# Kernel optimization log

Hardware: AMD Instinct MI355X
Metric: run time of the kernel (lower is better)

The kernel has to match this reference:

```python
import jax, jax.numpy as jnp
import numpy as np

WINDOW = 128
STRIDE = 16

def setup_inputs() -> dict:
    key = jax.random.key(0)
    input_data = jax.random.normal(key, (16, 4096, 128), dtype=jnp.float32)
    return {"input_data": input_data}

def reference(input_data) -> jnp.ndarray:
    B, T, F = input_data.shape
    num_windows = (T - WINDOW) // STRIDE + 1  # 249
    # time indices for every window: [num_windows, WINDOW]
    idx = jnp.arange(num_windows)[:, None] * STRIDE + jnp.arange(WINDOW)[None, :]
    # gather overlapping windows: [B, num_windows, WINDOW, F]
    windows = input_data[:, idx, :]
    # per-window X^T X / WINDOW: [B, num_windows, F, F]
    pccs = jnp.einsum('bwlf,bwlg->bwfg', windows, windows) / WINDOW
    return pccs
```

## Files before the change

kernel.cpp:

```cpp
#include <hip/hip_runtime.h>

#define WINDOW 128
#define STRIDE 16
#define NWIN   249
#define NF     128
#define SEQ    4096
#define LROWS  160

typedef _Float16 f16;
typedef _Float16 f16x2 __attribute__((ext_vector_type(2)));
typedef _Float16 f16x8 __attribute__((ext_vector_type(8)));
typedef float    f32x4 __attribute__((ext_vector_type(4)));
typedef float    f32x16 __attribute__((ext_vector_type(16)));

union V8 { f16x8 v8; f16x2 v2[4]; };

__device__ __forceinline__ void stage8(const float* __restrict__ src, f16* lds,
                                       int f0, int l0) {
    f32x4 rows[8];
    #pragma unroll
    for (int j = 0; j < 8; ++j)
        rows[j] = *(const f32x4*)&src[(size_t)(l0 + j) * NF + f0];
    const int cbase = l0 >> 3;
    #pragma unroll
    for (int d = 0; d < 4; ++d) {
        const int f = f0 + d;
        V8 u;
        #pragma unroll
        for (int jj = 0; jj < 4; ++jj) {
            auto p = __builtin_amdgcn_cvt_pkrtz(rows[2 * jj][d], rows[2 * jj + 1][d]);
            u.v2[jj] = *(f16x2*)&p;
        }
        u.v8 = u.v8 * (f16)0.08838834764831845f;
        const int ch = (l0 < 128) ? (cbase ^ (f & 15))
                                  : (16 + ((cbase & 3) ^ (f & 3)));
        *(f16x8*)&lds[f * LROWS + ch * 8] = u.v8;
    }
}

template<int CO>
__device__ __forceinline__ void compute_and_store(const f16* lds, int lane,
                                                  int wr, int wc, float* __restrict__ dst) {
    const int c15 = lane & 15;
    const int c31 = lane & 31;
    const int h   = lane >> 5;

    f32x16 acc[2][2];
    #pragma unroll
    for (int i = 0; i < 2; ++i)
        #pragma unroll
        for (int j = 0; j < 2; ++j)
            acc[i][j] = (f32x16)(0.0f);

    #pragma unroll
    for (int ks = 0; ks < 8; ++ks) {
        const int clog = CO + 2 * ks + h;
        int pc;
        if (CO == 0 || CO + 2 * ks + 1 < 16)
            pc = clog ^ c15;
        else
            pc = 16 + ((clog & 3) ^ (lane & 3));
        const int off = pc * 8;

        f16x8 af[2], bf[2];
        #pragma unroll
        for (int i = 0; i < 2; ++i)
            af[i] = *(const f16x8*)&lds[(64 * wr + 32 * i + c31) * LROWS + off];
        #pragma unroll
        for (int j = 0; j < 2; ++j)
            bf[j] = *(const f16x8*)&lds[(64 * wc + 32 * j + c31) * LROWS + off];

        #pragma unroll
        for (int i = 0; i < 2; ++i)
            #pragma unroll
            for (int j = 0; j < 2; ++j)
                acc[i][j] = __builtin_amdgcn_mfma_f32_32x32x16_f16(af[i], bf[j], acc[i][j], 0, 0, 0);
    }

    #pragma unroll
    for (int i = 0; i < 2; ++i) {
        const int R0 = 64 * wr + 32 * i + 4 * h;
        #pragma unroll
        for (int j = 0; j < 2; ++j) {
            float* dcol = dst + 64 * wc + 32 * j + c31;
            #pragma unroll
            for (int reg = 0; reg < 16; ++reg) {
                const int row = R0 + (reg & 3) + 8 * (reg >> 2);
                __builtin_nontemporal_store(acc[i][j][reg], &dcol[(size_t)row * NF]);
            }
        }
    }
}

__global__ __launch_bounds__(256, 4) void pcc_kernel(const float* __restrict__ in,
                                                     float* __restrict__ out) {
    __shared__ f16 lds[NF * LROWS];

    const int lin = blockIdx.x + 125 * blockIdx.y;
    const int swz = (lin & 7) * 250 + (lin >> 3);
    const int wp  = swz % 125;
    const int b   = swz / 125;

    const int tid = threadIdx.x;
    const bool full = (wp < 124);
    const int stage_base = full ? 32 * wp : (SEQ - 144);

    const float* src = in + ((size_t)b * SEQ + stage_base) * NF;
    const int f0 = 4 * (tid & 31);
    const int lh = tid >> 5;

    stage8(src, lds, f0, 8 * lh);
    stage8(src, lds, f0, 64 + 8 * lh);
    if (tid < 64)
        stage8(src, lds, f0, 128 + 8 * lh);
    __syncthreads();

    const int lane = tid & 63;
    const int wid  = tid >> 6;
    const int wr   = wid >> 1;
    const int wc   = wid & 1;

    float* outb = out + (size_t)b * NWIN * (NF * NF);
    if (full)
        compute_and_store<0>(lds, lane, wr, wc, outb + (size_t)(2 * wp) * (NF * NF));
    const int w1 = full ? (2 * wp + 1) : (NWIN - 1);
    compute_and_store<2>(lds, lane, wr, wc, outb + (size_t)w1 * (NF * NF));
}

extern "C" void kernel_launch(void* const* d_in, const int* in_sizes, int n_in,
                              void* d_out, int out_size, void* d_ws, size_t ws_size,
                              hipStream_t stream) {
    (void)in_sizes; (void)n_in; (void)d_ws; (void)ws_size; (void)out_size;
    const float* in = (const float*)d_in[0];
    float* out = (float*)d_out;
    dim3 grid(125, 16);
    pcc_kernel<<<grid, dim3(256, 1, 1), 0, stream>>>(in, out);
}
```

Measured before the change: 296.7 us.

## Process four windows per block using a ring LDS buffer with overlapped staging

Each block now covers a 64-row strip and computes four consecutive windows instead of two, staging 160 rows up front and then streaming the next 16 rows into a circular LDS buffer while earlier windows compute. This halves the number of blocks and reduces redundant global loads and f16 conversion of overlapping input rows. The LDS swizzle is simplified to XOR within groups of four chunks to support the wraparound. In exchange, the grid is smaller (63x16), which may lower occupancy and parallelism, and extra barriers are added inside the block.

```diff
diff --git a/kernel.cpp b/kernel.cpp
--- a/kernel.cpp
+++ b/kernel.cpp
@@ -6,22 +6,26 @@
 #define NF     128
 #define SEQ    4096
 #define LROWS  160
+#define NSTRIP 63
 
 typedef _Float16 f16;
 typedef _Float16 f16x2 __attribute__((ext_vector_type(2)));
+typedef _Float16 f16x4 __attribute__((ext_vector_type(4)));
 typedef _Float16 f16x8 __attribute__((ext_vector_type(8)));
 typedef float    f32x4 __attribute__((ext_vector_type(4)));
 typedef float    f32x16 __attribute__((ext_vector_type(16)));
 
 union V8 { f16x8 v8; f16x2 v2[4]; };
+union V4 { f16x4 v4; f16x2 v2[2]; };
+
 
 __device__ __forceinline__ void stage8(const float* __restrict__ src, f16* lds,
-                                       int f0, int l0) {
+                                       int f0, int l0 ) {
     f32x4 rows[8];
     #pragma unroll
     for (int j = 0; j < 8; ++j)
         rows[j] = *(const f32x4*)&src[(size_t)(l0 + j) * NF + f0];
-    const int cbase = l0 >> 3;
+    const int ch = l0 >> 3;
     #pragma unroll
     for (int d = 0; d < 4; ++d) {
         const int f = f0 + d;
@@ -32,18 +36,43 @@
             u.v2[jj] = *(f16x2*)&p;
         }
         u.v8 = u.v8 * (f16)0.08838834764831845f;
-        const int ch = (l0 < 128) ? (cbase ^ (f & 15))
-                                  : (16 + ((cbase & 3) ^ (f & 3)));
-        *(f16x8*)&lds[f * LROWS + ch * 8] = u.v8;
+        const int pch = (ch & ~3) | ((ch ^ (f >> 1)) & 3);
+        *(f16x8*)&lds[f * LROWS + pch * 8] = u.v8;
     }
 }
 
-template<int CO>
-__device__ __forceinline__ void compute_and_store(const f16* lds, int lane,
-                                                  int wr, int wc, float* __restrict__ dst) {
-    const int c15 = lane & 15;
+__device__ __forceinline__ void load4(const float* __restrict__ src, f32x4 r[4],
+                                      int f0, int l0) {
+    #pragma unroll
+    for (int j = 0; j < 4; ++j)
+        r[j] = *(const f32x4*)&src[(size_t)(l0 + j) * NF + f0];
+}
+
+__device__ __forceinline__ void write4(f16* lds, const f32x4 r[4], int f0, int relrow) {
+    const int phys = relrow - (relrow >= LROWS ? LROWS : 0);
+    const int ch = phys >> 3;
+    const int sub = phys & 7;
+    #pragma unroll
+    for (int d = 0; d < 4; ++d) {
+        const int f = f0 + d;
+        V4 u;
+        {
+            auto p0 = __builtin_amdgcn_cvt_pkrtz(r[0][d], r[1][d]);
+            auto p1 = __builtin_amdgcn_cvt_pkrtz(r[2][d], r[3][d]);
+            u.v2[0] = *(f16x2*)&p0;
+            u.v2[1] = *(f16x2*)&p1;
+        }
+        u.v4 = u.v4 * (f16)0.08838834764831845f;
+        const int pch = (ch & ~3) | ((ch ^ (f >> 1)) & 3);
+        *(f16x4*)&lds[f * LROWS + pch * 8 + sub] = u.v4;
+    }
+}
+
+__device__ __forceinline__ void compute_store(const f16* lds, int lane, int wr, int wc,
+                                              int wi, float* __restrict__ dst) {
     const int c31 = lane & 31;
     const int h   = lane >> 5;
+    const int q2  = c31 >> 1;
 
     f32x16 acc[2][2];
     #pragma unroll
@@ -52,29 +81,26 @@
         for (int j = 0; j < 2; ++j)
             acc[i][j] = (f32x16)(0.0f);
 
+    const int fa0 = (64 * wr + c31) * LROWS;
+    const int fa1 = (64 * wr + 32 + c31) * LROWS;
+    const int fb0 = (64 * wc + c31) * LROWS;
+    const int fb1 = (64 * wc + 32 + c31) * LROWS;
+
     #pragma unroll
     for (int ks = 0; ks < 8; ++ks) {
-        const int clog = CO + 2 * ks + h;
-        int pc;
-        if (CO == 0 || CO + 2 * ks + 1 < 16)
-            pc = clog ^ c15;
-        else
-            pc = 16 + ((clog & 3) ^ (lane & 3));
-        const int off = pc * 8;
+        const int chlog = 2 * wi + 2 * ks + h;
+        const int ch = chlog - (chlog >= 20 ? 20 : 0);
+        const int off = ((ch & ~3) | ((ch ^ q2) & 3)) * 8;
 
-        f16x8 af[2], bf[2];
-        #pragma unroll
-        for (int i = 0; i < 2; ++i)
-            af[i] = *(const f16x8*)&lds[(64 * wr + 32 * i + c31) * LROWS + off];
-        #pragma unroll
-        for (int j = 0; j < 2; ++j)
-            bf[j] = *(const f16x8*)&lds[(64 * wc + 32 * j + c31) * LROWS + off];
+        const f16x8 a0 = *(const f16x8*)&lds[fa0 + off];
+        const f16x8 a1 = *(const f16x8*)&lds[fa1 + off];
+        const f16x8 b0 = *(const f16x8*)&lds[fb0 + off];
+        const f16x8 b1 = *(const f16x8*)&lds[fb1 + off];
 
-        #pragma unroll
-        for (int i = 0; i < 2; ++i)
-            #pragma unroll
-            for (int j = 0; j < 2; ++j)
-                acc[i][j] = __builtin_amdgcn_mfma_f32_32x32x16_f16(af[i], bf[j], acc[i][j], 0, 0, 0);
+        acc[0][0] = __builtin_amdgcn_mfma_f32_32x32x16_f16(a0, b0, acc[0][0], 0, 0, 0);
+        acc[0][1] = __builtin_amdgcn_mfma_f32_32x32x16_f16(a0, b1, acc[0][1], 0, 0, 0);
+        acc[1][0] = __builtin_amdgcn_mfma_f32_32x32x16_f16(a1, b0, acc[1][0], 0, 0, 0);
+        acc[1][1] = __builtin_amdgcn_mfma_f32_32x32x16_f16(a1, b1, acc[1][1], 0, 0, 0);
     }
 
     #pragma unroll
@@ -96,22 +122,21 @@
                                                      float* __restrict__ out) {
     __shared__ f16 lds[NF * LROWS];
 
-    const int lin = blockIdx.x + 125 * blockIdx.y;
-    const int swz = (lin & 7) * 250 + (lin >> 3);
-    const int wp  = swz % 125;
-    const int b   = swz / 125;
+    const int lin  = blockIdx.x + NSTRIP * blockIdx.y;
+    const int swzb = (lin & 7) * 126 + (lin >> 3);
+    const int b    = swzb / NSTRIP;
+    const int s    = swzb - b * NSTRIP;
 
     const int tid = threadIdx.x;
-    const bool full = (wp < 124);
-    const int stage_base = full ? 32 * wp : (SEQ - 144);
-
-    const float* src = in + ((size_t)b * SEQ + stage_base) * NF;
+    const bool full = (s < NSTRIP - 1);
+    const int base = 64 * s;
+    const float* src = in + ((size_t)b * SEQ + base) * NF;
     const int f0 = 4 * (tid & 31);
     const int lh = tid >> 5;
 
     stage8(src, lds, f0, 8 * lh);
     stage8(src, lds, f0, 64 + 8 * lh);
-    if (tid < 64)
+    if (full && tid < 64)
         stage8(src, lds, f0, 128 + 8 * lh);
     __syncthreads();
 
@@ -120,11 +145,34 @@
     const int wr   = wid >> 1;
     const int wc   = wid & 1;
 
-    float* outb = out + (size_t)b * NWIN * (NF * NF);
-    if (full)
-        compute_and_store<0>(lds, lane, wr, wc, outb + (size_t)(2 * wp) * (NF * NF));
-    const int w1 = full ? (2 * wp + 1) : (NWIN - 1);
-    compute_and_store<2>(lds, lane, wr, wc, outb + (size_t)w1 * (NF * NF));
+    float* dst0 = out + (size_t)b * NWIN * (NF * NF) + (size_t)(4 * s) * (NF * NF);
+
+    if (!full) {
+        compute_store(lds, lane, wr, wc, 0, dst0);
+        return;
+    }
+
+    f32x4 hold[4];
+    const int r0 = 4 * lh;
+    load4(src, hold, f0, 144 + r0);
+
+    compute_store(lds, lane, wr, wc, 0, dst0);
+
+    __builtin_amdgcn_sched_barrier(0);
+    __builtin_amdgcn_s_barrier();
+    __builtin_amdgcn_sched_barrier(0);
+
+    write4(lds, hold, f0, 144 + r0);
+
+    compute_store(lds, lane, wr, wc, 1, dst0 + (size_t)(NF * NF));
+
+    asm volatile("s_waitcnt lgkmcnt(0)" ::: "memory");
+    __builtin_amdgcn_sched_barrier(0);
+    __builtin_amdgcn_s_barrier();
+    __builtin_amdgcn_sched_barrier(0);
+
+    compute_store(lds, lane, wr, wc, 2, dst0 + (size_t)2 * (NF * NF));
+    compute_store(lds, lane, wr, wc, 3, dst0 + (size_t)3 * (NF * NF));
 }
 
 extern "C" void kernel_launch(void* const* d_in, const int* in_sizes, int n_in,
@@ -133,6 +181,6 @@
     (void)in_sizes; (void)n_in; (void)d_ws; (void)ws_size; (void)out_size;
     const float* in = (const float*)d_in[0];
     float* out = (float*)d_out;
-    dim3 grid(125, 16);
+    dim3 grid(NSTRIP, 16);
     pcc_kernel<<<grid, dim3(256, 1, 1), 0, stream>>>(in, out);
 }
```

New measurement: 296.6 us. About the same (-0.0%).
